# Kernel tuning notes

Hardware: AMD Instinct MI355X
Metric: run time of the kernel (lower is better)

## Reference

```python
import jax, jax.numpy as jnp
import numpy as np

B, L, D = 2048, 200, 256
N_USERS, N_ATTRS, N_RATINGS = 100000, 50000, 5


def setup_inputs() -> dict:
    key = jax.random.key(0)
    ks = jax.random.split(key, 16)
    s = 0.02
    return {
        "nodes": jax.random.randint(ks[0], (B,), 0, N_USERS),
        "history_ua": jax.random.randint(ks[1], (B, L), 0, N_ATTRS),
        "history_r": jax.random.randint(ks[2], (B, L), 0, N_RATINGS),
        "history_uat": jax.random.randint(ks[3], (B, L), 0, 512),
        "u2e_w": jax.random.normal(ks[4], (N_USERS, D), jnp.float32) * s,
        "attr_w": jax.random.normal(ks[5], (N_ATTRS, D), jnp.float32) * s,
        "r2e_w": jax.random.normal(ks[6], (N_RATINGS, D), jnp.float32) * s,
        "w_r1_w": jax.random.normal(ks[7], (D, 2 * D), jnp.float32) * s,
        "w_r1_b": jnp.zeros((D,), jnp.float32),
        "w_r2_w": jax.random.normal(ks[8], (D, D), jnp.float32) * s,
        "w_r2_b": jnp.zeros((D,), jnp.float32),
        "att1_w": jax.random.normal(ks[9], (D, 2 * D), jnp.float32) * s,
        "att1_b": jnp.zeros((D,), jnp.float32),
        "att2_w": jax.random.normal(ks[10], (D, D), jnp.float32) * s,
        "att2_b": jnp.zeros((D,), jnp.float32),
        "att3_w": jax.random.normal(ks[11], (1, D), jnp.float32) * s,
        "att3_b": jnp.zeros((1,), jnp.float32),
    }


def reference(nodes, history_ua, history_r, history_uat,
              u2e_w, attr_w, r2e_w,
              w_r1_w, w_r1_b, w_r2_w, w_r2_b,
              att1_w, att1_b, att2_w, att2_b, att3_w, att3_b):
    # gathers: e_ua [B,L,D], e_r [B,L,D], ua_rep [B,D]
    e_ua = attr_w[history_ua]
    e_r = r2e_w[history_r]
    ua_rep = u2e_w[nodes]
    # o_history = relu(w_r2(relu(w_r1(cat(e_ua, e_r)))))  [B,L,D]
    x = jnp.concatenate([e_ua, e_r], axis=-1)            # [B,L,2D]
    x = jax.nn.relu(jnp.einsum('bld,kd->blk', x, w_r1_w) + w_r1_b)
    o = jax.nn.relu(jnp.einsum('bld,kd->blk', x, w_r2_w) + w_r2_b)
    # attention: MLP on cat(o_history, ua_rep) -> softmax over history dim
    a = jnp.concatenate([o, jnp.broadcast_to(ua_rep[:, None, :], o.shape)], axis=-1)  # [B,L,2D]
    h = jax.nn.relu(jnp.einsum('bld,kd->blk', a, att1_w) + att1_b)
    h = jax.nn.relu(jnp.einsum('bld,kd->blk', h, att2_w) + att2_b)
    score = jnp.einsum('bld,kd->blk', h, att3_w) + att3_b  # [B,L,1]
    att = jax.nn.softmax(score, axis=1)
    # weighted reduce: o^T @ att per node -> [B,D]
    return jnp.sum(o * att, axis=1)
```

## Files before the change

### kernel.cpp

```cpp
#include <hip/hip_runtime.h>
#include <hip/hip_bf16.h>

typedef __bf16 bf16;
typedef __bf16 bf16x8 __attribute__((ext_vector_type(8)));
typedef float f32x4 __attribute__((ext_vector_type(4)));

#define L_SZ 200
#define D_SZ 256
#define NROWS (2048 * 200)
#define MB 128
#define AST 264
#define N_ATTR 50000

#define WS_W2F 0u
#define WS_A1L 131072u
#define WS_A1H 262144u
#define WS_A2F 393216u
#define WS_W1A 524288u
#define WS_W1F 655360u
#define WS_R   917504u
#define WS_H1P 925696u
#define WS_SCR 3022848u
#define WS_O   4661248u
#define WS_P   214376448u
#define WS_NEED_OLD 214376448u
#define WS_NEED_NEW 239976448u

__global__ void swizzle_kernel(const float* __restrict__ W, bf16* __restrict__ dst,
                               int KT, int ldw, int koff, int total) {
    int g = blockIdx.x * blockDim.x + threadIdx.x;
    if (g >= total) return;
    int lane = g & 63;
    int kt = (g >> 6) % KT;
    int nt = g / (64 * KT);
    int n = nt * 16 + (lane & 15);
    int k = kt * 32 + (lane >> 4) * 8;
    const float* src = W + (long)n * ldw + koff + k;
    f32x4 a = *(const f32x4*)src;
    f32x4 b = *(const f32x4*)(src + 4);
    bf16x8 v;
    v[0] = (bf16)a[0]; v[1] = (bf16)a[1]; v[2] = (bf16)a[2]; v[3] = (bf16)a[3];
    v[4] = (bf16)b[0]; v[5] = (bf16)b[1]; v[6] = (bf16)b[2]; v[7] = (bf16)b[3];
    *(bf16x8*)(dst + (long)g * 8) = v;
}

__device__ __forceinline__ void stage_rows(const int* __restrict__ idxl,
                                           const float* __restrict__ table,
                                           bf16* __restrict__ buf, int t) {
#pragma unroll
    for (int it = 0; it < 16; ++it) {
        int g = it * 256 + t;
        int r = g >> 5;
        int c = g & 31;
        long row = idxl[r];
        const float* f = table + row * D_SZ + c * 8;
        f32x4 a = *(const f32x4*)f;
        f32x4 b = *(const f32x4*)(f + 4);
        bf16x8 v;
        v[0] = (bf16)a[0]; v[1] = (bf16)a[1]; v[2] = (bf16)a[2]; v[3] = (bf16)a[3];
        v[4] = (bf16)b[0]; v[5] = (bf16)b[1]; v[6] = (bf16)b[2]; v[7] = (bf16)b[3];
        *(bf16x8*)(buf + r * AST + c * 8) = v;
    }
}

template <int KTOT>
__device__ __forceinline__ void gemm8(const bf16* __restrict__ abase,
                                      const bf16* __restrict__ wfrag, int koff_t,
                                      int wave, int lane, int l16, int quad,
                                      f32x4 acc[8][4]) {
    const bf16* wbase = wfrag + ((long)(wave * 4) * KTOT + koff_t) * 512 + lane * 8;
    bf16x8 bc[4], bn[4];
#pragma unroll
    for (int nt = 0; nt < 4; ++nt)
        bc[nt] = *(const bf16x8*)(wbase + (long)nt * KTOT * 512);
#pragma unroll
    for (int kt = 0; kt < 8; ++kt) {
        if (kt < 7) {
#pragma unroll
            for (int nt = 0; nt < 4; ++nt)
                bn[nt] = *(const bf16x8*)(wbase + ((long)nt * KTOT + kt + 1) * 512);
        }
        bf16x8 a[8];
#pragma unroll
        for (int mt = 0; mt < 8; ++mt)
            a[mt] = *(const bf16x8*)(abase + (mt * 16 + l16) * AST + kt * 32 + quad * 8);
#pragma unroll
        for (int nt = 0; nt < 4; ++nt)
#pragma unroll
            for (int mt = 0; mt < 8; ++mt)
                acc[mt][nt] = __builtin_amdgcn_mfma_f32_16x16x32_bf16(a[mt], bc[nt], acc[mt][nt], 0, 0, 0);
#pragma unroll
        for (int nt = 0; nt < 4; ++nt) bc[nt] = bn[nt];
    }
}

__device__ __forceinline__ void zero8(f32x4 acc[8][4]) {
    f32x4 z = {0.f, 0.f, 0.f, 0.f};
#pragma unroll
    for (int mt = 0; mt < 8; ++mt)
#pragma unroll
        for (int nt = 0; nt < 4; ++nt) acc[mt][nt] = z;
}

__device__ __forceinline__ void store_act8(bf16* __restrict__ buf, f32x4 acc[8][4],
                                           const float* bias, int wave, int l16, int quad) {
#pragma unroll
    for (int mt = 0; mt < 8; ++mt)
#pragma unroll
        for (int nt = 0; nt < 4; ++nt) {
            int col = (wave * 4 + nt) * 16 + l16;
#pragma unroll
            for (int r = 0; r < 4; ++r) {
                int row = mt * 16 + quad * 4 + r;
                float v = acc[mt][nt][r] + bias[nt];
                v = v > 0.f ? v : 0.f;
                buf[row * AST + col] = (bf16)v;
            }
        }
}

__device__ __forceinline__ void store_lin8(bf16* __restrict__ buf, f32x4 acc[8][4],
                                           int wave, int l16, int quad) {
#pragma unroll
    for (int mt = 0; mt < 8; ++mt)
#pragma unroll
        for (int nt = 0; nt < 4; ++nt) {
            int col = (wave * 4 + nt) * 16 + l16;
#pragma unroll
            for (int r = 0; r < 4; ++r) {
                int row = mt * 16 + quad * 4 + r;
                buf[row * AST + col] = (bf16)acc[mt][nt][r];
            }
        }
}

__global__ void kR_bias(const float* __restrict__ w1, const float* __restrict__ r2e,
                        const float* __restrict__ b1w, float* __restrict__ Rg) {
    __shared__ float e[5 * D_SZ];
    const int t = threadIdx.x;
    for (int i = t; i < 5 * D_SZ; i += 256) e[i] = r2e[i];
    __syncthreads();
    const float* wr = w1 + (long)t * 512 + 256;
    float bb = b1w[t];
    for (int r = 0; r < 5; ++r) {
        float a = bb;
        const float* er = e + r * D_SZ;
#pragma unroll
        for (int k = 0; k < D_SZ; k += 4) {
            f32x4 wv = *(const f32x4*)(wr + k);
            a += er[k] * wv[0] + er[k + 1] * wv[1] + er[k + 2] * wv[2] + er[k + 3] * wv[3];
        }
        Rg[r * D_SZ + t] = a;
    }
}

__launch_bounds__(256, 2)
__global__ void kpre_P(const float* __restrict__ attr, const bf16* __restrict__ wf_w1a,
                       bf16* __restrict__ Pt) {
    __shared__ __align__(16) bf16 abuf[MB * AST];
    __shared__ int idxl[MB];
    const int blk = blockIdx.x, t = threadIdx.x;
    const int wave = t >> 6, lane = t & 63, l16 = t & 15, quad = (t & 63) >> 4;
    if (t < MB) { int r = blk * MB + t; idxl[t] = r < N_ATTR ? r : (N_ATTR - 1); }
    __syncthreads();
    stage_rows(idxl, attr, abuf, t);
    __syncthreads();
    f32x4 acc[8][4];
    zero8(acc);
    gemm8<8>(abuf, wf_w1a, 0, wave, lane, l16, quad, acc);
    __syncthreads();
    store_lin8(abuf, acc, wave, l16, quad);
    __syncthreads();
#pragma unroll
    for (int it = 0; it < 16; ++it) {
        int g = it * 256 + t;
        int r = g >> 5, c = g & 31;
        long row = (long)blk * MB + r;
        if (row < N_ATTR)
            *(bf16x8*)(Pt + row * D_SZ + c * 8) = *(const bf16x8*)(abuf + r * AST + c * 8);
    }
}

__launch_bounds__(256, 2)
__global__ void k0_h1pre(const int* __restrict__ nodes, const float* __restrict__ u2e,
                         const bf16* __restrict__ wf_a1h, const float* __restrict__ a1b,
                         float* __restrict__ h1p) {
    __shared__ __align__(16) bf16 abuf[MB * AST];
    __shared__ int idxl[MB];
    const int blk = blockIdx.x, t = threadIdx.x;
    const int wave = t >> 6, lane = t & 63, l16 = t & 15, quad = (t & 63) >> 4;
    if (t < MB) idxl[t] = nodes[blk * MB + t];
    __syncthreads();
    stage_rows(idxl, u2e, abuf, t);
    __syncthreads();
    f32x4 acc[8][4];
    zero8(acc);
    gemm8<8>(abuf, wf_a1h, 0, wave, lane, l16, quad, acc);
#pragma unroll
    for (int nt = 0; nt < 4; ++nt) {
        int col = (wave * 4 + nt) * 16 + l16;
        float ab = a1b[col];
#pragma unroll
        for (int mt = 0; mt < 8; ++mt)
#pragma unroll
            for (int r = 0; r < 4; ++r) {
                int row = mt * 16 + quad * 4 + r;
                h1p[(long)(blk * MB + row) * D_SZ + col] = acc[mt][nt][r] + ab;
            }
    }
}

__launch_bounds__(256, 2)
__global__ void k1f_fused(const int* __restrict__ hua, const int* __restrict__ hr,
                          const bf16* __restrict__ Pt, const float* __restrict__ Rg,
                          const bf16* __restrict__ wf_w2, const bf16* __restrict__ wf_a1l,
                          const bf16* __restrict__ wf_a2f, const float* __restrict__ h1p,
                          const float* __restrict__ b2w, const float* __restrict__ a2b,
                          const float* __restrict__ a3w,
                          bf16* __restrict__ o_out, float* __restrict__ scores) {
    __shared__ __align__(16) bf16 abuf[MB * AST];
    __shared__ int idx_ua[MB], idx_r[MB];
    __shared__ float Rl[5 * D_SZ];
    __shared__ float hp[2][D_SZ];
    __shared__ float spart[4][MB];
    const int blk = blockIdx.x, t = threadIdx.x;
    const int wave = t >> 6, lane = t & 63, l16 = t & 15, quad = (t & 63) >> 4;
    const long r0 = (long)blk * MB;
    const int b0 = (int)(r0 / L_SZ);
    const int b1i = min(b0 + 1, 2047);
    const long bsplit = (long)(b0 + 1) * L_SZ;
    if (t < MB) { idx_ua[t] = hua[r0 + t]; idx_r[t] = hr[r0 + t]; }
    for (int i = t; i < 5 * D_SZ; i += 256) Rl[i] = Rg[i];
    hp[0][t] = h1p[(long)b0 * D_SZ + t];
    hp[1][t] = h1p[(long)b1i * D_SZ + t];
    __syncthreads();
#pragma unroll
    for (int it = 0; it < 8; ++it) {
        int g = it * 256 + t;
        int r = g >> 4, c = g & 15;
        long row = idx_ua[r];
        const bf16* pp = Pt + row * D_SZ + c * 16;
        bf16x8 v0 = *(const bf16x8*)pp;
        bf16x8 v1 = *(const bf16x8*)(pp + 8);
        const float* Rr = Rl + idx_r[r] * D_SZ + c * 16;
        f32x4 ra = *(const f32x4*)(Rr);
        f32x4 rb = *(const f32x4*)(Rr + 4);
        f32x4 rc = *(const f32x4*)(Rr + 8);
        f32x4 rd = *(const f32x4*)(Rr + 12);
        bf16x8 o0, o1;
#pragma unroll
        for (int j = 0; j < 4; ++j) {
            float a = (float)v0[j] + ra[j];
            float b = (float)v0[j + 4] + rb[j];
            float cc = (float)v1[j] + rc[j];
            float d = (float)v1[j + 4] + rd[j];
            o0[j]     = (bf16)(a > 0.f ? a : 0.f);
            o0[j + 4] = (bf16)(b > 0.f ? b : 0.f);
            o1[j]     = (bf16)(cc > 0.f ? cc : 0.f);
            o1[j + 4] = (bf16)(d > 0.f ? d : 0.f);
        }
        *(bf16x8*)(abuf + r * AST + c * 16) = o0;
        *(bf16x8*)(abuf + r * AST + c * 16 + 8) = o1;
    }
    __syncthreads();

    float bias2[4], bias4[4], a3[4];
#pragma unroll
    for (int nt = 0; nt < 4; ++nt) {
        int col = (wave * 4 + nt) * 16 + l16;
        bias2[nt] = b2w[col];
        bias4[nt] = a2b[col];
        a3[nt] = a3w[col];
    }

    f32x4 acc[8][4];
    zero8(acc);
    gemm8<8>(abuf, wf_w2, 0, wave, lane, l16, quad, acc);
    __syncthreads();
    store_act8(abuf, acc, bias2, wave, l16, quad);
    __syncthreads();
#pragma unroll
    for (int it = 0; it < 16; ++it) {
        int g = it * 256 + t;
        int r = g >> 5, c = g & 31;
        *(bf16x8*)(o_out + (r0 + r) * D_SZ + c * 8) = *(const bf16x8*)(abuf + r * AST + c * 8);
    }
    zero8(acc);
    gemm8<8>(abuf, wf_a1l, 0, wave, lane, l16, quad, acc);
    __syncthreads();
#pragma unroll
    for (int nt = 0; nt < 4; ++nt) {
        int col = (wave * 4 + nt) * 16 + l16;
#pragma unroll
        for (int mt = 0; mt < 8; ++mt)
#pragma unroll
            for (int r = 0; r < 4; ++r) {
                int row = mt * 16 + quad * 4 + r;
                float bias = ((r0 + row) >= bsplit) ? hp[1][col] : hp[0][col];
                float v = acc[mt][nt][r] + bias;
                v = v > 0.f ? v : 0.f;
                abuf[row * AST + col] = (bf16)v;
            }
    }
    __syncthreads();
    zero8(acc);
    gemm8<8>(abuf, wf_a2f, 0, wave, lane, l16, quad, acc);

    float p[8][4];
#pragma unroll
    for (int mt = 0; mt < 8; ++mt)
#pragma unroll
        for (int r = 0; r < 4; ++r) {
            float s = 0.f;
#pragma unroll
            for (int nt = 0; nt < 4; ++nt) {
                float h = acc[mt][nt][r] + bias4[nt];
                h = h > 0.f ? h : 0.f;
                s += h * a3[nt];
            }
            p[mt][r] = s;
        }
#pragma unroll
    for (int off = 1; off < 16; off <<= 1)
#pragma unroll
        for (int mt = 0; mt < 8; ++mt)
#pragma unroll
            for (int r = 0; r < 4; ++r) p[mt][r] += __shfl_xor(p[mt][r], off, 16);
    if (l16 == 0) {
#pragma unroll
        for (int mt = 0; mt < 8; ++mt)
#pragma unroll
            for (int r = 0; r < 4; ++r)
                spart[wave][mt * 16 + quad * 4 + r] = p[mt][r];
    }
    __syncthreads();
    if (t < MB)
        scores[r0 + t] = spart[0][t] + spart[1][t] + spart[2][t] + spart[3][t];
}

__launch_bounds__(256, 2)
__global__ void k1_gemm12(const int* __restrict__ hua, const int* __restrict__ hr,
                          const float* __restrict__ attr, const float* __restrict__ r2e,
                          const bf16* __restrict__ wf_w1, const bf16* __restrict__ wf_w2,
                          const float* __restrict__ b1w, const float* __restrict__ b2w,
                          bf16* __restrict__ o_out) {
    __shared__ __align__(16) bf16 abuf[MB * AST];
    __shared__ int idx_ua[MB], idx_r[MB];
    const int blk = blockIdx.x, t = threadIdx.x;
    const int wave = t >> 6, lane = t & 63, l16 = t & 15, quad = (t & 63) >> 4;
    const long r0 = (long)blk * MB;
    if (t < MB) { idx_ua[t] = hua[r0 + t]; idx_r[t] = hr[r0 + t]; }
    __syncthreads();

    float bias1[4], bias2[4];
#pragma unroll
    for (int nt = 0; nt < 4; ++nt) {
        int col = (wave * 4 + nt) * 16 + l16;
        bias1[nt] = b1w[col];
        bias2[nt] = b2w[col];
    }

    f32x4 acc[8][4];
    zero8(acc);
    stage_rows(idx_ua, attr, abuf, t);
    __syncthreads();
    gemm8<16>(abuf, wf_w1, 0, wave, lane, l16, quad, acc);
    __syncthreads();
    stage_rows(idx_r, r2e, abuf, t);
    __syncthreads();
    gemm8<16>(abuf, wf_w1, 8, wave, lane, l16, quad, acc);
    __syncthreads();
    store_act8(abuf, acc, bias1, wave, l16, quad);
    __syncthreads();
    zero8(acc);
    gemm8<8>(abuf, wf_w2, 0, wave, lane, l16, quad, acc);
    __syncthreads();
    store_act8(abuf, acc, bias2, wave, l16, quad);
    __syncthreads();
#pragma unroll
    for (int it = 0; it < 16; ++it) {
        int g = it * 256 + t;
        int r = g >> 5, c = g & 31;
        *(bf16x8*)(o_out + (r0 + r) * D_SZ + c * 8) = *(const bf16x8*)(abuf + r * AST + c * 8);
    }
}

__launch_bounds__(256, 2)
__global__ void k2_gemm34(const bf16* __restrict__ o_in,
                          const bf16* __restrict__ wf_a1l, const bf16* __restrict__ wf_a2f,
                          const float* __restrict__ h1p, const float* __restrict__ a2b,
                          const float* __restrict__ a3w, float* __restrict__ scores) {
    __shared__ __align__(16) bf16 abuf[MB * AST];
    __shared__ float hp[2][D_SZ];
    __shared__ float spart[4][MB];
    const int blk = blockIdx.x, t = threadIdx.x;
    const int wave = t >> 6, lane = t & 63, l16 = t & 15, quad = (t & 63) >> 4;
    const long r0 = (long)blk * MB;
    const int b0 = (int)(r0 / L_SZ);
    const int b1 = min(b0 + 1, 2047);
    const long bsplit = (long)(b0 + 1) * L_SZ;
    hp[0][t] = h1p[(long)b0 * D_SZ + t];
    hp[1][t] = h1p[(long)b1 * D_SZ + t];
#pragma unroll
    for (int it = 0; it < 16; ++it) {
        int g = it * 256 + t;
        int r = g >> 5, c = g & 31;
        *(bf16x8*)(abuf + r * AST + c * 8) = *(const bf16x8*)(o_in + (r0 + r) * D_SZ + c * 8);
    }
    __syncthreads();

    f32x4 acc[8][4];
    zero8(acc);
    gemm8<8>(abuf, wf_a1l, 0, wave, lane, l16, quad, acc);
    __syncthreads();
#pragma unroll
    for (int nt = 0; nt < 4; ++nt) {
        int col = (wave * 4 + nt) * 16 + l16;
#pragma unroll
        for (int mt = 0; mt < 8; ++mt)
#pragma unroll
            for (int r = 0; r < 4; ++r) {
                int row = mt * 16 + quad * 4 + r;
                float bias = ((r0 + row) >= bsplit) ? hp[1][col] : hp[0][col];
                float v = acc[mt][nt][r] + bias;
                v = v > 0.f ? v : 0.f;
                abuf[row * AST + col] = (bf16)v;
            }
    }
    __syncthreads();
    zero8(acc);
    gemm8<8>(abuf, wf_a2f, 0, wave, lane, l16, quad, acc);

    float bias4[4], a3[4];
#pragma unroll
    for (int nt = 0; nt < 4; ++nt) {
        int col = (wave * 4 + nt) * 16 + l16;
        bias4[nt] = a2b[col];
        a3[nt] = a3w[col];
    }
    float p[8][4];
#pragma unroll
    for (int mt = 0; mt < 8; ++mt)
#pragma unroll
        for (int r = 0; r < 4; ++r) {
            float s = 0.f;
#pragma unroll
            for (int nt = 0; nt < 4; ++nt) {
                float h = acc[mt][nt][r] + bias4[nt];
                h = h > 0.f ? h : 0.f;
                s += h * a3[nt];
            }
            p[mt][r] = s;
        }
#pragma unroll
    for (int off = 1; off < 16; off <<= 1)
#pragma unroll
        for (int mt = 0; mt < 8; ++mt)
#pragma unroll
            for (int r = 0; r < 4; ++r) p[mt][r] += __shfl_xor(p[mt][r], off, 16);
    if (l16 == 0) {
#pragma unroll
        for (int mt = 0; mt < 8; ++mt)
#pragma unroll
            for (int r = 0; r < 4; ++r)
                spart[wave][mt * 16 + quad * 4 + r] = p[mt][r];
    }
    __syncthreads();
    if (t < MB)
        scores[r0 + t] = spart[0][t] + spart[1][t] + spart[2][t] + spart[3][t];
}

__global__ void k5_reduce(const float* __restrict__ scores, const bf16* __restrict__ o_in,
                          float* __restrict__ out) {
    __shared__ float red[256];
    __shared__ float watt[256];
    const int b = blockIdx.x, t = threadIdx.x;
    float s = (t < L_SZ) ? scores[(long)b * L_SZ + t] : -INFINITY;
    red[t] = s;
    __syncthreads();
    for (int off = 128; off > 0; off >>= 1) {
        if (t < off) red[t] = fmaxf(red[t], red[t + off]);
        __syncthreads();
    }
    float mx = red[0];
    __syncthreads();
    float w = (t < L_SZ) ? __expf(s - mx) : 0.f;
    watt[t] = w;
    red[t] = w;
    __syncthreads();
    for (int off = 128; off > 0; off >>= 1) {
        if (t < off) red[t] += red[t + off];
        __syncthreads();
    }
    float inv = 1.f / red[0];
    float accv = 0.f;
    const bf16* ob = o_in + (long)b * L_SZ * D_SZ + t;
#pragma unroll 4
    for (int l = 0; l < L_SZ; ++l) accv += watt[l] * (float)ob[(long)l * D_SZ];
    out[(long)b * D_SZ + t] = accv * inv;
}

__device__ __forceinline__ void gather_half_f(const int* __restrict__ idxp,
                                              const float* __restrict__ table,
                                              bf16* __restrict__ buf, int l0, int t) {
#pragma unroll
    for (int it = 0; it < 6; ++it) {
        int g = it * 256 + t;
        int r = g >> 5, c = g & 31;
        int l = l0 + r;
        int li = l < L_SZ ? l : (L_SZ - 1);
        long row = idxp[li];
        const float* f = table + row * D_SZ + c * 8;
        f32x4 a = *(const f32x4*)f;
        f32x4 b2 = *(const f32x4*)(f + 4);
        bf16x8 v;
        v[0] = (bf16)a[0]; v[1] = (bf16)a[1]; v[2] = (bf16)a[2]; v[3] = (bf16)a[3];
        v[4] = (bf16)b2[0]; v[5] = (bf16)b2[1]; v[6] = (bf16)b2[2]; v[7] = (bf16)b2[3];
        *(bf16x8*)(buf + r * AST + c * 8) = v;
    }
}

template <int KTOT>
__device__ __forceinline__ void run_gemm3(const bf16* __restrict__ abase,
                                          const bf16* __restrict__ wfrag, int koff_t,
                                          int wave, int lane, int l16, int quad,
                                          f32x4 acc[3][4]) {
    const bf16* wbase = wfrag + ((long)(wave * 4) * KTOT + koff_t) * 512 + lane * 8;
    bf16x8 bc[4], bn[4];
#pragma unroll
    for (int nt = 0; nt < 4; ++nt)
        bc[nt] = *(const bf16x8*)(wbase + (long)nt * KTOT * 512);
#pragma unroll
    for (int kt = 0; kt < 8; ++kt) {
        if (kt < 7) {
#pragma unroll
            for (int nt = 0; nt < 4; ++nt)
                bn[nt] = *(const bf16x8*)(wbase + ((long)nt * KTOT + kt + 1) * 512);
        }
        bf16x8 a[3];
#pragma unroll
        for (int mt = 0; mt < 3; ++mt)
            a[mt] = *(const bf16x8*)(abase + (mt * 16 + l16) * AST + kt * 32 + quad * 8);
#pragma unroll
        for (int nt = 0; nt < 4; ++nt)
#pragma unroll
            for (int mt = 0; mt < 3; ++mt)
                acc[mt][nt] = __builtin_amdgcn_mfma_f32_16x16x32_bf16(a[mt], bc[nt], acc[mt][nt], 0, 0, 0);
#pragma unroll
        for (int nt = 0; nt < 4; ++nt) bc[nt] = bn[nt];
    }
}

__launch_bounds__(256, 3)
__global__ void ua_fused(const int* __restrict__ nodes, const int* __restrict__ hua,
                         const int* __restrict__ hr, const float* __restrict__ u2e,
                         const float* __restrict__ attr, const float* __restrict__ r2e,
                         const bf16* __restrict__ wf1, const bf16* __restrict__ wf2,
                         const bf16* __restrict__ wfa1, const bf16* __restrict__ wfa2,
                         const float* __restrict__ b1w, const float* __restrict__ b2w,
                         const float* __restrict__ att1w, const float* __restrict__ a1b,
                         const float* __restrict__ a2b, const float* __restrict__ att3w,
                         const float* __restrict__ a3bp, float* __restrict__ out) {
    __shared__ __align__(16) bf16 abuf[48 * AST];
    __shared__ __align__(16) bf16 obuf[48 * AST];
    __shared__ float h1pre[D_SZ];
    __shared__ float scratch[288];
    const int b = blockIdx.x, t = threadIdx.x;
    const int wave = t >> 6, lane = t & 63, l16 = t & 15, quad = (t & 63) >> 4;
    {
        int node = nodes[b];
        scratch[t] = u2e[(long)node * D_SZ + t];
        __syncthreads();
        float a = a1b[t];
        const float* wr = att1w + (long)t * 512 + 256;
#pragma unroll
        for (int k = 0; k < 256; k += 4) {
            f32x4 wv = *(const f32x4*)(wr + k);
            a += scratch[k] * wv[0] + scratch[k + 1] * wv[1] +
                 scratch[k + 2] * wv[2] + scratch[k + 3] * wv[3];
        }
        h1pre[t] = a;
        __syncthreads();
    }
    float bias1[4], bias2[4], bias3[4], bias4[4], a3[4];
#pragma unroll
    for (int nt = 0; nt < 4; ++nt) {
        int col = (wave * 4 + nt) * 16 + l16;
        bias1[nt] = b1w[col]; bias2[nt] = b2w[col]; bias3[nt] = h1pre[col];
        bias4[nt] = a2b[col]; a3[nt] = att3w[col];
    }
    const float a3bias = a3bp[0];
    const int* huab = hua + (long)b * L_SZ;
    const int* hrb = hr + (long)b * L_SZ;
    float accv = 0.f, srun = 0.f, mrun = -INFINITY;
    float* score_part = scratch;
    float* score_row = scratch + 192;
    float* wrow = scratch + 240;
    auto st3 = [&](bf16* buf, f32x4 acc[3][4], const float* bias) {
#pragma unroll
        for (int mt = 0; mt < 3; ++mt)
#pragma unroll
            for (int nt = 0; nt < 4; ++nt) {
                int col = (wave * 4 + nt) * 16 + l16;
#pragma unroll
                for (int r = 0; r < 4; ++r) {
                    float v = acc[mt][nt][r] + bias[nt];
                    v = v > 0.f ? v : 0.f;
                    buf[(mt * 16 + quad * 4 + r) * AST + col] = (bf16)v;
                }
            }
    };
    for (int tile = 0; tile < 5; ++tile) {
        const int l0 = tile * 48;
        f32x4 acc[3][4];
        f32x4 z = {0.f, 0.f, 0.f, 0.f};
#pragma unroll
        for (int mt = 0; mt < 3; ++mt)
#pragma unroll
            for (int nt = 0; nt < 4; ++nt) acc[mt][nt] = z;
        gather_half_f(huab, attr, abuf, l0, t);
        __syncthreads();
        run_gemm3<16>(abuf, wf1, 0, wave, lane, l16, quad, acc);
        __syncthreads();
        gather_half_f(hrb, r2e, abuf, l0, t);
        __syncthreads();
        run_gemm3<16>(abuf, wf1, 8, wave, lane, l16, quad, acc);
        __syncthreads();
        st3(abuf, acc, bias1);
        __syncthreads();
#pragma unroll
        for (int mt = 0; mt < 3; ++mt)
#pragma unroll
            for (int nt = 0; nt < 4; ++nt) acc[mt][nt] = z;
        run_gemm3<8>(abuf, wf2, 0, wave, lane, l16, quad, acc);
        st3(obuf, acc, bias2);
        __syncthreads();
#pragma unroll
        for (int mt = 0; mt < 3; ++mt)
#pragma unroll
            for (int nt = 0; nt < 4; ++nt) acc[mt][nt] = z;
        run_gemm3<8>(obuf, wfa1, 0, wave, lane, l16, quad, acc);
        st3(abuf, acc, bias3);
        __syncthreads();
#pragma unroll
        for (int mt = 0; mt < 3; ++mt)
#pragma unroll
            for (int nt = 0; nt < 4; ++nt) acc[mt][nt] = z;
        run_gemm3<8>(abuf, wfa2, 0, wave, lane, l16, quad, acc);
        float p[3][4];
#pragma unroll
        for (int mt = 0; mt < 3; ++mt)
#pragma unroll
            for (int r = 0; r < 4; ++r) {
                float s = 0.f;
#pragma unroll
                for (int nt = 0; nt < 4; ++nt) {
                    float h = acc[mt][nt][r] + bias4[nt];
                    h = h > 0.f ? h : 0.f;
                    s += h * a3[nt];
                }
                p[mt][r] = s;
            }
#pragma unroll
        for (int off = 1; off < 16; off <<= 1)
#pragma unroll
            for (int mt = 0; mt < 3; ++mt)
#pragma unroll
                for (int r = 0; r < 4; ++r) p[mt][r] += __shfl_xor(p[mt][r], off, 16);
        if (l16 == 0) {
#pragma unroll
            for (int mt = 0; mt < 3; ++mt)
#pragma unroll
                for (int r = 0; r < 4; ++r)
                    score_part[wave * 48 + mt * 16 + quad * 4 + r] = p[mt][r];
        }
        __syncthreads();
        if (t < 48) {
            float s = score_part[t] + score_part[48 + t] + score_part[96 + t] +
                      score_part[144 + t] + a3bias;
            score_row[t] = (l0 + t < L_SZ) ? s : -INFINITY;
        }
        __syncthreads();
        float tm = -INFINITY;
        for (int r = 0; r < 48; ++r) tm = fmaxf(tm, score_row[r]);
        float nm = fmaxf(mrun, tm);
        float factor = __expf(mrun - nm);
        if (t < 48) wrow[t] = __expf(score_row[t] - nm);
        __syncthreads();
        float wsum = 0.f, av = 0.f;
#pragma unroll 8
        for (int r = 0; r < 48; ++r) {
            float w = wrow[r];
            wsum += w;
            av += w * (float)obuf[r * AST + t];
        }
        accv = accv * factor + av;
        srun = srun * factor + wsum;
        mrun = nm;
        __syncthreads();
    }
    out[(long)b * D_SZ + t] = accv / srun;
}

extern "C" void kernel_launch(void* const* d_in, const int* in_sizes, int n_in,
                              void* d_out, int out_size, void* d_ws, size_t ws_size,
                              hipStream_t stream) {
    const int* nodes = (const int*)d_in[0];
    const int* hua = (const int*)d_in[1];
    const int* hr = (const int*)d_in[2];
    const float* u2e = (const float*)d_in[4];
    const float* attr = (const float*)d_in[5];
    const float* r2e = (const float*)d_in[6];
    const float* w1 = (const float*)d_in[7];
    const float* b1 = (const float*)d_in[8];
    const float* w2 = (const float*)d_in[9];
    const float* b2 = (const float*)d_in[10];
    const float* a1w = (const float*)d_in[11];
    const float* a1b = (const float*)d_in[12];
    const float* a2w = (const float*)d_in[13];
    const float* a2b = (const float*)d_in[14];
    const float* a3w = (const float*)d_in[15];
    const float* a3b = (const float*)d_in[16];
    char* ws = (char*)d_ws;
    bf16* wf_w2 = (bf16*)(ws + WS_W2F);
    bf16* wf_a1l = (bf16*)(ws + WS_A1L);
    bf16* wf_a1h = (bf16*)(ws + WS_A1H);
    bf16* wf_a2f = (bf16*)(ws + WS_A2F);
    bf16* wf_w1a = (bf16*)(ws + WS_W1A);
    bf16* wf_w1 = (bf16*)(ws + WS_W1F);

    swizzle_kernel<<<32, 256, 0, stream>>>(w2, wf_w2, 8, 256, 0, 8192);
    swizzle_kernel<<<32, 256, 0, stream>>>(a1w, wf_a1l, 8, 512, 0, 8192);
    swizzle_kernel<<<32, 256, 0, stream>>>(a2w, wf_a2f, 8, 256, 0, 8192);

    if (ws_size >= (size_t)WS_NEED_NEW) {
        float* Rg = (float*)(ws + WS_R);
        float* h1p = (float*)(ws + WS_H1P);
        float* scores = (float*)(ws + WS_SCR);
        bf16* obuf = (bf16*)(ws + WS_O);
        bf16* Pt = (bf16*)(ws + WS_P);
        swizzle_kernel<<<32, 256, 0, stream>>>(a1w, wf_a1h, 8, 512, 256, 8192);
        swizzle_kernel<<<32, 256, 0, stream>>>(w1, wf_w1a, 8, 512, 0, 8192);
        kR_bias<<<1, 256, 0, stream>>>(w1, r2e, b1, Rg);
        kpre_P<<<(N_ATTR + MB - 1) / MB, 256, 0, stream>>>(attr, wf_w1a, Pt);
        k0_h1pre<<<2048 / MB, 256, 0, stream>>>(nodes, u2e, wf_a1h, a1b, h1p);
        k1f_fused<<<NROWS / MB, 256, 0, stream>>>(hua, hr, Pt, Rg, wf_w2, wf_a1l,
                                                  wf_a2f, h1p, b2, a2b, a3w,
                                                  obuf, scores);
        k5_reduce<<<2048, 256, 0, stream>>>(scores, obuf, (float*)d_out);
    } else if (ws_size >= (size_t)WS_NEED_OLD) {
        float* h1p = (float*)(ws + WS_H1P);
        float* scores = (float*)(ws + WS_SCR);
        bf16* obuf = (bf16*)(ws + WS_O);
        swizzle_kernel<<<64, 256, 0, stream>>>(w1, wf_w1, 16, 512, 0, 16384);
        swizzle_kernel<<<32, 256, 0, stream>>>(a1w, wf_a1h, 8, 512, 256, 8192);
        k0_h1pre<<<2048 / MB, 256, 0, stream>>>(nodes, u2e, wf_a1h, a1b, h1p);
        k1_gemm12<<<NROWS / MB, 256, 0, stream>>>(hua, hr, attr, r2e, wf_w1, wf_w2,
                                                  b1, b2, obuf);
        k2_gemm34<<<NROWS / MB, 256, 0, stream>>>(obuf, wf_a1l, wf_a2f, h1p, a2b,
                                                  a3w, scores);
        k5_reduce<<<2048, 256, 0, stream>>>(scores, obuf, (float*)d_out);
    } else {
        swizzle_kernel<<<64, 256, 0, stream>>>(w1, wf_w1, 16, 512, 0, 16384);
        ua_fused<<<2048, 256, 0, stream>>>(nodes, hua, hr, u2e, attr, r2e,
                                           wf_w1, wf_w2, wf_a1l, wf_a2f,
                                           b1, b2, a1w, a1b, a2b, a3w, a3b,
                                           (float*)d_out);
    }
}
```

Baseline: 614.6 us.

## Halve fused tile rows, merge prep kernels, and vectorize the weighted reduce

The main fused kernel now processes 64 rows per block instead of 128, with launch bounds raised to 4 blocks per CU. This shrinks LDS and accumulator registers so more blocks can be resident. The five swizzle launches and the R-bias kernel are merged into one launch, and the P-precompute and user-projection kernels are merged into another, cutting launch overhead. The final reduce reads bf16x8 vectors across 8 row groups and combines them through shared memory, replacing the strided scalar loads. Smaller tiles mean each weight fragment is reused over fewer rows, so weight traffic per output row doubles.

```diff
diff --git a/kernel.cpp b/kernel.cpp
--- a/kernel.cpp
+++ b/kernel.cpp
@@ -9,8 +9,10 @@
 #define D_SZ 256
 #define NROWS (2048 * 200)
 #define MB 128
+#define MB2 64
 #define AST 264
 #define N_ATTR 50000
+#define NPB ((N_ATTR + MB - 1) / MB)
 
 #define WS_W2F 0u
 #define WS_A1L 131072u
@@ -26,10 +28,8 @@
 #define WS_NEED_OLD 214376448u
 #define WS_NEED_NEW 239976448u
 
-__global__ void swizzle_kernel(const float* __restrict__ W, bf16* __restrict__ dst,
-                               int KT, int ldw, int koff, int total) {
-    int g = blockIdx.x * blockDim.x + threadIdx.x;
-    if (g >= total) return;
+__device__ __forceinline__ void swz_one(const float* __restrict__ W, bf16* __restrict__ dst,
+                                        int KT, int ldw, int koff, int g) {
     int lane = g & 63;
     int kt = (g >> 6) % KT;
     int nt = g / (64 * KT);
@@ -44,6 +44,52 @@
     *(bf16x8*)(dst + (long)g * 8) = v;
 }
 
+__global__ void swizzle_kernel(const float* __restrict__ W, bf16* __restrict__ dst,
+                               int KT, int ldw, int koff, int total) {
+    int g = blockIdx.x * blockDim.x + threadIdx.x;
+    if (g >= total) return;
+    swz_one(W, dst, KT, ldw, koff, g);
+}
+
+__global__ void swizzle_all(const float* __restrict__ w2, const float* __restrict__ a1w,
+                            const float* __restrict__ a2w, const float* __restrict__ w1,
+                            bf16* __restrict__ wf_w2, bf16* __restrict__ wf_a1l,
+                            bf16* __restrict__ wf_a2f, bf16* __restrict__ wf_a1h,
+                            bf16* __restrict__ wf_w1a,
+                            const float* __restrict__ r2e, const float* __restrict__ b1w,
+                            float* __restrict__ Rg) {
+    __shared__ float e[5 * D_SZ];
+    const int blk = blockIdx.x, t = threadIdx.x;
+    if (blk == 160) {
+        for (int i = t; i < 5 * D_SZ; i += 256) e[i] = r2e[i];
+        __syncthreads();
+        const float* wr = w1 + (long)t * 512 + 256;
+        float bb = b1w[t];
+        for (int r = 0; r < 5; ++r) {
+            float a = bb;
+            const float* er = e + r * D_SZ;
+#pragma unroll
+            for (int k = 0; k < D_SZ; k += 4) {
+                f32x4 wv = *(const f32x4*)(wr + k);
+                a += er[k] * wv[0] + er[k + 1] * wv[1] + er[k + 2] * wv[2] + er[k + 3] * wv[3];
+            }
+            Rg[r * D_SZ + t] = a;
+        }
+        return;
+    }
+    int job = blk >> 5, lb = blk & 31;
+    int g = lb * 256 + t;
+    const float* W; bf16* dst; int ldw, koff;
+    switch (job) {
+        case 0:  W = w2;  dst = wf_w2;  ldw = 256; koff = 0;   break;
+        case 1:  W = a1w; dst = wf_a1l; ldw = 512; koff = 0;   break;
+        case 2:  W = a2w; dst = wf_a2f; ldw = 256; koff = 0;   break;
+        case 3:  W = a1w; dst = wf_a1h; ldw = 512; koff = 256; break;
+        default: W = w1;  dst = wf_w1a; ldw = 512; koff = 0;   break;
+    }
+    swz_one(W, dst, 8, ldw, koff, g);
+}
+
 __device__ __forceinline__ void stage_rows(const int* __restrict__ idxl,
                                            const float* __restrict__ table,
                                            bf16* __restrict__ buf, int t) {
@@ -63,11 +109,11 @@
     }
 }
 
-template <int KTOT>
-__device__ __forceinline__ void gemm8(const bf16* __restrict__ abase,
-                                      const bf16* __restrict__ wfrag, int koff_t,
-                                      int wave, int lane, int l16, int quad,
-                                      f32x4 acc[8][4]) {
+template <int MT, int KTOT>
+__device__ __forceinline__ void gemm_t(const bf16* __restrict__ abase,
+                                       const bf16* __restrict__ wfrag, int koff_t,
+                                       int wave, int lane, int l16, int quad,
+                                       f32x4 (&acc)[MT][4]) {
     const bf16* wbase = wfrag + ((long)(wave * 4) * KTOT + koff_t) * 512 + lane * 8;
     bf16x8 bc[4], bn[4];
 #pragma unroll
@@ -80,32 +126,34 @@
             for (int nt = 0; nt < 4; ++nt)
                 bn[nt] = *(const bf16x8*)(wbase + ((long)nt * KTOT + kt + 1) * 512);
         }
-        bf16x8 a[8];
-#pragma unroll
-        for (int mt = 0; mt < 8; ++mt)
+        bf16x8 a[MT];
+#pragma unroll
+        for (int mt = 0; mt < MT; ++mt)
             a[mt] = *(const bf16x8*)(abase + (mt * 16 + l16) * AST + kt * 32 + quad * 8);
 #pragma unroll
         for (int nt = 0; nt < 4; ++nt)
 #pragma unroll
-            for (int mt = 0; mt < 8; ++mt)
+            for (int mt = 0; mt < MT; ++mt)
                 acc[mt][nt] = __builtin_amdgcn_mfma_f32_16x16x32_bf16(a[mt], bc[nt], acc[mt][nt], 0, 0, 0);
 #pragma unroll
         for (int nt = 0; nt < 4; ++nt) bc[nt] = bn[nt];
     }
 }
 
-__device__ __forceinline__ void zero8(f32x4 acc[8][4]) {
+template <int MT>
+__device__ __forceinline__ void zero_t(f32x4 (&acc)[MT][4]) {
     f32x4 z = {0.f, 0.f, 0.f, 0.f};
 #pragma unroll
-    for (int mt = 0; mt < 8; ++mt)
+    for (int mt = 0; mt < MT; ++mt)
 #pragma unroll
         for (int nt = 0; nt < 4; ++nt) acc[mt][nt] = z;
 }
 
-__device__ __forceinline__ void store_act8(bf16* __restrict__ buf, f32x4 acc[8][4],
-                                           const float* bias, int wave, int l16, int quad) {
-#pragma unroll
-    for (int mt = 0; mt < 8; ++mt)
+template <int MT>
+__device__ __forceinline__ void store_act_t(bf16* __restrict__ buf, f32x4 (&acc)[MT][4],
+                                            const float* bias, int wave, int l16, int quad) {
+#pragma unroll
+    for (int mt = 0; mt < MT; ++mt)
 #pragma unroll
         for (int nt = 0; nt < 4; ++nt) {
             int col = (wave * 4 + nt) * 16 + l16;
@@ -119,7 +167,7 @@
         }
 }
 
-__device__ __forceinline__ void store_lin8(bf16* __restrict__ buf, f32x4 acc[8][4],
+__device__ __forceinline__ void store_lin8(bf16* __restrict__ buf, f32x4 (&acc)[8][4],
                                            int wave, int l16, int quad) {
 #pragma unroll
     for (int mt = 0; mt < 8; ++mt)
@@ -134,50 +182,53 @@
         }
 }
 
-__global__ void kR_bias(const float* __restrict__ w1, const float* __restrict__ r2e,
-                        const float* __restrict__ b1w, float* __restrict__ Rg) {
-    __shared__ float e[5 * D_SZ];
-    const int t = threadIdx.x;
-    for (int i = t; i < 5 * D_SZ; i += 256) e[i] = r2e[i];
-    __syncthreads();
-    const float* wr = w1 + (long)t * 512 + 256;
-    float bb = b1w[t];
-    for (int r = 0; r < 5; ++r) {
-        float a = bb;
-        const float* er = e + r * D_SZ;
-#pragma unroll
-        for (int k = 0; k < D_SZ; k += 4) {
-            f32x4 wv = *(const f32x4*)(wr + k);
-            a += er[k] * wv[0] + er[k + 1] * wv[1] + er[k + 2] * wv[2] + er[k + 3] * wv[3];
-        }
-        Rg[r * D_SZ + t] = a;
-    }
-}
-
 __launch_bounds__(256, 2)
-__global__ void kpre_P(const float* __restrict__ attr, const bf16* __restrict__ wf_w1a,
-                       bf16* __restrict__ Pt) {
+__global__ void kpre_k0(const float* __restrict__ attr, const bf16* __restrict__ wf_w1a,
+                        bf16* __restrict__ Pt,
+                        const int* __restrict__ nodes, const float* __restrict__ u2e,
+                        const bf16* __restrict__ wf_a1h, const float* __restrict__ a1b,
+                        float* __restrict__ h1p) {
     __shared__ __align__(16) bf16 abuf[MB * AST];
     __shared__ int idxl[MB];
     const int blk = blockIdx.x, t = threadIdx.x;
     const int wave = t >> 6, lane = t & 63, l16 = t & 15, quad = (t & 63) >> 4;
-    if (t < MB) { int r = blk * MB + t; idxl[t] = r < N_ATTR ? r : (N_ATTR - 1); }
-    __syncthreads();
-    stage_rows(idxl, attr, abuf, t);
+    const bool isP = blk < NPB;
+    if (t < MB) {
+        if (isP) { int r = blk * MB + t; idxl[t] = r < N_ATTR ? r : (N_ATTR - 1); }
+        else idxl[t] = nodes[(blk - NPB) * MB + t];
+    }
+    __syncthreads();
+    stage_rows(idxl, isP ? attr : u2e, abuf, t);
     __syncthreads();
     f32x4 acc[8][4];
-    zero8(acc);
-    gemm8<8>(abuf, wf_w1a, 0, wave, lane, l16, quad, acc);
-    __syncthreads();
-    store_lin8(abuf, acc, wave, l16, quad);
-    __syncthreads();
-#pragma unroll
-    for (int it = 0; it < 16; ++it) {
-        int g = it * 256 + t;
-        int r = g >> 5, c = g & 31;
-        long row = (long)blk * MB + r;
-        if (row < N_ATTR)
-            *(bf16x8*)(Pt + row * D_SZ + c * 8) = *(const bf16x8*)(abuf + r * AST + c * 8);
+    zero_t<8>(acc);
+    gemm_t<8, 8>(abuf, isP ? wf_w1a : wf_a1h, 0, wave, lane, l16, quad, acc);
+    if (isP) {
+        __syncthreads();
+        store_lin8(abuf, acc, wave, l16, quad);
+        __syncthreads();
+#pragma unroll
+        for (int it = 0; it < 16; ++it) {
+            int g = it * 256 + t;
+            int r = g >> 5, c = g & 31;
+            long row = (long)blk * MB + r;
+            if (row < N_ATTR)
+                *(bf16x8*)(Pt + row * D_SZ + c * 8) = *(const bf16x8*)(abuf + r * AST + c * 8);
+        }
+    } else {
+        const int blk0 = blk - NPB;
+#pragma unroll
+        for (int nt = 0; nt < 4; ++nt) {
+            int col = (wave * 4 + nt) * 16 + l16;
+            float ab = a1b[col];
+#pragma unroll
+            for (int mt = 0; mt < 8; ++mt)
+#pragma unroll
+                for (int r = 0; r < 4; ++r) {
+                    int row = mt * 16 + quad * 4 + r;
+                    h1p[(long)(blk0 * MB + row) * D_SZ + col] = acc[mt][nt][r] + ab;
+                }
+        }
     }
 }
 
@@ -194,8 +245,8 @@
     stage_rows(idxl, u2e, abuf, t);
     __syncthreads();
     f32x4 acc[8][4];
-    zero8(acc);
-    gemm8<8>(abuf, wf_a1h, 0, wave, lane, l16, quad, acc);
+    zero_t<8>(acc);
+    gemm_t<8, 8>(abuf, wf_a1h, 0, wave, lane, l16, quad, acc);
 #pragma unroll
     for (int nt = 0; nt < 4; ++nt) {
         int col = (wave * 4 + nt) * 16 + l16;
@@ -210,7 +261,7 @@
     }
 }
 
-__launch_bounds__(256, 2)
+__launch_bounds__(256, 4)
 __global__ void k1f_fused(const int* __restrict__ hua, const int* __restrict__ hr,
                           const bf16* __restrict__ Pt, const float* __restrict__ Rg,
                           const bf16* __restrict__ wf_w2, const bf16* __restrict__ wf_a1l,
@@ -218,24 +269,21 @@
                           const float* __restrict__ b2w, const float* __restrict__ a2b,
                           const float* __restrict__ a3w,
                           bf16* __restrict__ o_out, float* __restrict__ scores) {
-    __shared__ __align__(16) bf16 abuf[MB * AST];
-    __shared__ int idx_ua[MB], idx_r[MB];
+    __shared__ __align__(16) bf16 abuf[MB2 * AST];
+    __shared__ int idx_ua[MB2], idx_r[MB2];
     __shared__ float Rl[5 * D_SZ];
-    __shared__ float hp[2][D_SZ];
-    __shared__ float spart[4][MB];
+    __shared__ float spart[4][MB2];
     const int blk = blockIdx.x, t = threadIdx.x;
     const int wave = t >> 6, lane = t & 63, l16 = t & 15, quad = (t & 63) >> 4;
-    const long r0 = (long)blk * MB;
+    const long r0 = (long)blk * MB2;
     const int b0 = (int)(r0 / L_SZ);
     const int b1i = min(b0 + 1, 2047);
     const long bsplit = (long)(b0 + 1) * L_SZ;
-    if (t < MB) { idx_ua[t] = hua[r0 + t]; idx_r[t] = hr[r0 + t]; }
+    if (t < MB2) { idx_ua[t] = hua[r0 + t]; idx_r[t] = hr[r0 + t]; }
     for (int i = t; i < 5 * D_SZ; i += 256) Rl[i] = Rg[i];
-    hp[0][t] = h1p[(long)b0 * D_SZ + t];
-    hp[1][t] = h1p[(long)b1i * D_SZ + t];
-    __syncthreads();
-#pragma unroll
-    for (int it = 0; it < 8; ++it) {
+    __syncthreads();
+#pragma unroll
+    for (int it = 0; it < 4; ++it) {
         int g = it * 256 + t;
         int r = g >> 4, c = g & 15;
         long row = idx_ua[r];
@@ -264,51 +312,59 @@
     }
     __syncthreads();
 
-    float bias2[4], bias4[4], a3[4];
-#pragma unroll
-    for (int nt = 0; nt < 4; ++nt) {
-        int col = (wave * 4 + nt) * 16 + l16;
-        bias2[nt] = b2w[col];
-        bias4[nt] = a2b[col];
-        a3[nt] = a3w[col];
-    }
-
-    f32x4 acc[8][4];
-    zero8(acc);
-    gemm8<8>(abuf, wf_w2, 0, wave, lane, l16, quad, acc);
-    __syncthreads();
-    store_act8(abuf, acc, bias2, wave, l16, quad);
-    __syncthreads();
-#pragma unroll
-    for (int it = 0; it < 16; ++it) {
+    f32x4 acc[4][4];
+    zero_t<4>(acc);
+    gemm_t<4, 8>(abuf, wf_w2, 0, wave, lane, l16, quad, acc);
+    __syncthreads();
+    float bias2[4];
+#pragma unroll
+    for (int nt = 0; nt < 4; ++nt) bias2[nt] = b2w[(wave * 4 + nt) * 16 + l16];
+    store_act_t<4>(abuf, acc, bias2, wave, l16, quad);
+    __syncthreads();
+#pragma unroll
+    for (int it = 0; it < 8; ++it) {
         int g = it * 256 + t;
         int r = g >> 5, c = g & 31;
         *(bf16x8*)(o_out + (r0 + r) * D_SZ + c * 8) = *(const bf16x8*)(abuf + r * AST + c * 8);
     }
-    zero8(acc);
-    gemm8<8>(abuf, wf_a1l, 0, wave, lane, l16, quad, acc);
-    __syncthreads();
+    zero_t<4>(acc);
+    gemm_t<4, 8>(abuf, wf_a1l, 0, wave, lane, l16, quad, acc);
+    __syncthreads();
+    float h0v[4], h1v[4];
 #pragma unroll
     for (int nt = 0; nt < 4; ++nt) {
         int col = (wave * 4 + nt) * 16 + l16;
-#pragma unroll
-        for (int mt = 0; mt < 8; ++mt)
+        h0v[nt] = h1p[(long)b0 * D_SZ + col];
+        h1v[nt] = h1p[(long)b1i * D_SZ + col];
+    }
+#pragma unroll
+    for (int nt = 0; nt < 4; ++nt) {
+        int col = (wave * 4 + nt) * 16 + l16;
+#pragma unroll
+        for (int mt = 0; mt < 4; ++mt)
 #pragma unroll
             for (int r = 0; r < 4; ++r) {
                 int row = mt * 16 + quad * 4 + r;
-                float bias = ((r0 + row) >= bsplit) ? hp[1][col] : hp[0][col];
+                float bias = ((r0 + row) >= bsplit) ? h1v[nt] : h0v[nt];
                 float v = acc[mt][nt][r] + bias;
                 v = v > 0.f ? v : 0.f;
                 abuf[row * AST + col] = (bf16)v;
             }
     }
     __syncthreads();
-    zero8(acc);
-    gemm8<8>(abuf, wf_a2f, 0, wave, lane, l16, quad, acc);
-
-    float p[8][4];
-#pragma unroll
-    for (int mt = 0; mt < 8; ++mt)
+    zero_t<4>(acc);
+    gemm_t<4, 8>(abuf, wf_a2f, 0, wave, lane, l16, quad, acc);
+
+    float bias4[4], a3[4];
+#pragma unroll
+    for (int nt = 0; nt < 4; ++nt) {
+        int col = (wave * 4 + nt) * 16 + l16;
+        bias4[nt] = a2b[col];
+        a3[nt] = a3w[col];
+    }
+    float p[4][4];
+#pragma unroll
+    for (int mt = 0; mt < 4; ++mt)
 #pragma unroll
         for (int r = 0; r < 4; ++r) {
             float s = 0.f;
@@ -323,18 +379,18 @@
 #pragma unroll
     for (int off = 1; off < 16; off <<= 1)
 #pragma unroll
-        for (int mt = 0; mt < 8; ++mt)
+        for (int mt = 0; mt < 4; ++mt)
 #pragma unroll
             for (int r = 0; r < 4; ++r) p[mt][r] += __shfl_xor(p[mt][r], off, 16);
     if (l16 == 0) {
 #pragma unroll
-        for (int mt = 0; mt < 8; ++mt)
+        for (int mt = 0; mt < 4; ++mt)
 #pragma unroll
             for (int r = 0; r < 4; ++r)
                 spart[wave][mt * 16 + quad * 4 + r] = p[mt][r];
     }
     __syncthreads();
-    if (t < MB)
+    if (t < MB2)
         scores[r0 + t] = spart[0][t] + spart[1][t] + spart[2][t] + spart[3][t];
 }
 
@@ -361,21 +417,21 @@
     }
 
     f32x4 acc[8][4];
-    zero8(acc);
+    zero_t<8>(acc);
     stage_rows(idx_ua, attr, abuf, t);
     __syncthreads();
-    gemm8<16>(abuf, wf_w1, 0, wave, lane, l16, quad, acc);
+    gemm_t<8, 16>(abuf, wf_w1, 0, wave, lane, l16, quad, acc);
     __syncthreads();
     stage_rows(idx_r, r2e, abuf, t);
     __syncthreads();
-    gemm8<16>(abuf, wf_w1, 8, wave, lane, l16, quad, acc);
-    __syncthreads();
-    store_act8(abuf, acc, bias1, wave, l16, quad);
-    __syncthreads();
-    zero8(acc);
-    gemm8<8>(abuf, wf_w2, 0, wave, lane, l16, quad, acc);
-    __syncthreads();
-    store_act8(abuf, acc, bias2, wave, l16, quad);
+    gemm_t<8, 16>(abuf, wf_w1, 8, wave, lane, l16, quad, acc);
+    __syncthreads();
+    store_act_t<8>(abuf, acc, bias1, wave, l16, quad);
+    __syncthreads();
+    zero_t<8>(acc);
+    gemm_t<8, 8>(abuf, wf_w2, 0, wave, lane, l16, quad, acc);
+    __syncthreads();
+    store_act_t<8>(abuf, acc, bias2, wave, l16, quad);
     __syncthreads();
 #pragma unroll
     for (int it = 0; it < 16; ++it) {
@@ -410,8 +466,8 @@
     __syncthreads();
 
     f32x4 acc[8][4];
-    zero8(acc);
-    gemm8<8>(abuf, wf_a1l, 0, wave, lane, l16, quad, acc);
+    zero_t<8>(acc);
+    gemm_t<8, 8>(abuf, wf_a1l, 0, wave, lane, l16, quad, acc);
     __syncthreads();
 #pragma unroll
     for (int nt = 0; nt < 4; ++nt) {
@@ -428,8 +484,8 @@
             }
     }
     __syncthreads();
-    zero8(acc);
-    gemm8<8>(abuf, wf_a2f, 0, wave, lane, l16, quad, acc);
+    zero_t<8>(acc);
+    gemm_t<8, 8>(abuf, wf_a2f, 0, wave, lane, l16, quad, acc);
 
     float bias4[4], a3[4];
 #pragma unroll
@@ -474,6 +530,7 @@
                           float* __restrict__ out) {
     __shared__ float red[256];
     __shared__ float watt[256];
+    __shared__ float racc[8][264];
     const int b = blockIdx.x, t = threadIdx.x;
     float s = (t < L_SZ) ? scores[(long)b * L_SZ + t] : -INFINITY;
     red[t] = s;
@@ -493,11 +550,25 @@
         __syncthreads();
     }
     float inv = 1.f / red[0];
-    float accv = 0.f;
-    const bf16* ob = o_in + (long)b * L_SZ * D_SZ + t;
-#pragma unroll 4
-    for (int l = 0; l < L_SZ; ++l) accv += watt[l] * (float)ob[(long)l * D_SZ];
-    out[(long)b * D_SZ + t] = accv * inv;
+    const int c8 = t & 31, rg = t >> 5;
+    f32x4 a0 = {0.f, 0.f, 0.f, 0.f}, a1 = {0.f, 0.f, 0.f, 0.f};
+    const bf16* ob = o_in + (long)b * L_SZ * D_SZ + c8 * 8;
+#pragma unroll 5
+    for (int l = rg; l < L_SZ; l += 8) {
+        float wv = watt[l];
+        bf16x8 v = *(const bf16x8*)(ob + (long)l * D_SZ);
+        a0[0] += wv * (float)v[0]; a0[1] += wv * (float)v[1];
+        a0[2] += wv * (float)v[2]; a0[3] += wv * (float)v[3];
+        a1[0] += wv * (float)v[4]; a1[1] += wv * (float)v[5];
+        a1[2] += wv * (float)v[6]; a1[3] += wv * (float)v[7];
+    }
+    *(f32x4*)(&racc[rg][c8 * 8]) = a0;
+    *(f32x4*)(&racc[rg][c8 * 8 + 4]) = a1;
+    __syncthreads();
+    float r2 = 0.f;
+#pragma unroll
+    for (int g = 0; g < 8; ++g) r2 += racc[g][t];
+    out[(long)b * D_SZ + t] = r2 * inv;
 }
 
 __device__ __forceinline__ void gather_half_f(const int* __restrict__ idxp,
@@ -517,37 +588,6 @@
         v[0] = (bf16)a[0]; v[1] = (bf16)a[1]; v[2] = (bf16)a[2]; v[3] = (bf16)a[3];
         v[4] = (bf16)b2[0]; v[5] = (bf16)b2[1]; v[6] = (bf16)b2[2]; v[7] = (bf16)b2[3];
         *(bf16x8*)(buf + r * AST + c * 8) = v;
-    }
-}
-
-template <int KTOT>
-__device__ __forceinline__ void run_gemm3(const bf16* __restrict__ abase,
-                                          const bf16* __restrict__ wfrag, int koff_t,
-                                          int wave, int lane, int l16, int quad,
-                                          f32x4 acc[3][4]) {
-    const bf16* wbase = wfrag + ((long)(wave * 4) * KTOT + koff_t) * 512 + lane * 8;
-    bf16x8 bc[4], bn[4];
-#pragma unroll
-    for (int nt = 0; nt < 4; ++nt)
-        bc[nt] = *(const bf16x8*)(wbase + (long)nt * KTOT * 512);
-#pragma unroll
-    for (int kt = 0; kt < 8; ++kt) {
-        if (kt < 7) {
-#pragma unroll
-            for (int nt = 0; nt < 4; ++nt)
-                bn[nt] = *(const bf16x8*)(wbase + ((long)nt * KTOT + kt + 1) * 512);
-        }
-        bf16x8 a[3];
-#pragma unroll
-        for (int mt = 0; mt < 3; ++mt)
-            a[mt] = *(const bf16x8*)(abase + (mt * 16 + l16) * AST + kt * 32 + quad * 8);
-#pragma unroll
-        for (int nt = 0; nt < 4; ++nt)
-#pragma unroll
-            for (int mt = 0; mt < 3; ++mt)
-                acc[mt][nt] = __builtin_amdgcn_mfma_f32_16x16x32_bf16(a[mt], bc[nt], acc[mt][nt], 0, 0, 0);
-#pragma unroll
-        for (int nt = 0; nt < 4; ++nt) bc[nt] = bn[nt];
     }
 }
 
@@ -596,7 +636,7 @@
     float* score_part = scratch;
     float* score_row = scratch + 192;
     float* wrow = scratch + 240;
-    auto st3 = [&](bf16* buf, f32x4 acc[3][4], const float* bias) {
+    auto st3 = [&](bf16* buf, f32x4 (&acc)[3][4], const float* bias) {
 #pragma unroll
         for (int mt = 0; mt < 3; ++mt)
 #pragma unroll
@@ -613,40 +653,27 @@
     for (int tile = 0; tile < 5; ++tile) {
         const int l0 = tile * 48;
         f32x4 acc[3][4];
-        f32x4 z = {0.f, 0.f, 0.f, 0.f};
-#pragma unroll
-        for (int mt = 0; mt < 3; ++mt)
-#pragma unroll
-            for (int nt = 0; nt < 4; ++nt) acc[mt][nt] = z;
+        zero_t<3>(acc);
         gather_half_f(huab, attr, abuf, l0, t);
         __syncthreads();
-        run_gemm3<16>(abuf, wf1, 0, wave, lane, l16, quad, acc);
+        gemm_t<3, 16>(abuf, wf1, 0, wave, lane, l16, quad, acc);
         __syncthreads();
         gather_half_f(hrb, r2e, abuf, l0, t);
         __syncthreads();
-        run_gemm3<16>(abuf, wf1, 8, wave, lane, l16, quad, acc);
+        gemm_t<3, 16>(abuf, wf1, 8, wave, lane, l16, quad, acc);
         __syncthreads();
         st3(abuf, acc, bias1);
         __syncthreads();
-#pragma unroll
-        for (int mt = 0; mt < 3; ++mt)
-#pragma unroll
-            for (int nt = 0; nt < 4; ++nt) acc[mt][nt] = z;
-        run_gemm3<8>(abuf, wf2, 0, wave, lane, l16, quad, acc);
+        zero_t<3>(acc);
+        gemm_t<3, 8>(abuf, wf2, 0, wave, lane, l16, quad, acc);
         st3(obuf, acc, bias2);
         __syncthreads();
-#pragma unroll
-        for (int mt = 0; mt < 3; ++mt)
-#pragma unroll
-            for (int nt = 0; nt < 4; ++nt) acc[mt][nt] = z;
-        run_gemm3<8>(obuf, wfa1, 0, wave, lane, l16, quad, acc);
+        zero_t<3>(acc);
+        gemm_t<3, 8>(obuf, wfa1, 0, wave, lane, l16, quad, acc);
         st3(abuf, acc, bias3);
         __syncthreads();
-#pragma unroll
-        for (int mt = 0; mt < 3; ++mt)
-#pragma unroll
-            for (int nt = 0; nt < 4; ++nt) acc[mt][nt] = z;
-        run_gemm3<8>(abuf, wfa2, 0, wave, lane, l16, quad, acc);
+        zero_t<3>(acc);
+        gemm_t<3, 8>(abuf, wfa2, 0, wave, lane, l16, quad, acc);
         float p[3][4];
 #pragma unroll
         for (int mt = 0; mt < 3; ++mt)
@@ -729,29 +756,28 @@
     bf16* wf_w1a = (bf16*)(ws + WS_W1A);
     bf16* wf_w1 = (bf16*)(ws + WS_W1F);
 
-    swizzle_kernel<<<32, 256, 0, stream>>>(w2, wf_w2, 8, 256, 0, 8192);
-    swizzle_kernel<<<32, 256, 0, stream>>>(a1w, wf_a1l, 8, 512, 0, 8192);
-    swizzle_kernel<<<32, 256, 0, stream>>>(a2w, wf_a2f, 8, 256, 0, 8192);
-
     if (ws_size >= (size_t)WS_NEED_NEW) {
         float* Rg = (float*)(ws + WS_R);
         float* h1p = (float*)(ws + WS_H1P);
         float* scores = (float*)(ws + WS_SCR);
         bf16* obuf = (bf16*)(ws + WS_O);
         bf16* Pt = (bf16*)(ws + WS_P);
-        swizzle_kernel<<<32, 256, 0, stream>>>(a1w, wf_a1h, 8, 512, 256, 8192);
-        swizzle_kernel<<<32, 256, 0, stream>>>(w1, wf_w1a, 8, 512, 0, 8192);
-        kR_bias<<<1, 256, 0, stream>>>(w1, r2e, b1, Rg);
-        kpre_P<<<(N_ATTR + MB - 1) / MB, 256, 0, stream>>>(attr, wf_w1a, Pt);
-        k0_h1pre<<<2048 / MB, 256, 0, stream>>>(nodes, u2e, wf_a1h, a1b, h1p);
-        k1f_fused<<<NROWS / MB, 256, 0, stream>>>(hua, hr, Pt, Rg, wf_w2, wf_a1l,
-                                                  wf_a2f, h1p, b2, a2b, a3w,
-                                                  obuf, scores);
+        swizzle_all<<<161, 256, 0, stream>>>(w2, a1w, a2w, w1,
+                                             wf_w2, wf_a1l, wf_a2f, wf_a1h, wf_w1a,
+                                             r2e, b1, Rg);
+        kpre_k0<<<NPB + 2048 / MB, 256, 0, stream>>>(attr, wf_w1a, Pt,
+                                                     nodes, u2e, wf_a1h, a1b, h1p);
+        k1f_fused<<<NROWS / MB2, 256, 0, stream>>>(hua, hr, Pt, Rg, wf_w2, wf_a1l,
+                                                   wf_a2f, h1p, b2, a2b, a3w,
+                                                   obuf, scores);
         k5_reduce<<<2048, 256, 0, stream>>>(scores, obuf, (float*)d_out);
     } else if (ws_size >= (size_t)WS_NEED_OLD) {
         float* h1p = (float*)(ws + WS_H1P);
         float* scores = (float*)(ws + WS_SCR);
         bf16* obuf = (bf16*)(ws + WS_O);
+        swizzle_kernel<<<32, 256, 0, stream>>>(w2, wf_w2, 8, 256, 0, 8192);
+        swizzle_kernel<<<32, 256, 0, stream>>>(a1w, wf_a1l, 8, 512, 0, 8192);
+        swizzle_kernel<<<32, 256, 0, stream>>>(a2w, wf_a2f, 8, 256, 0, 8192);
         swizzle_kernel<<<64, 256, 0, stream>>>(w1, wf_w1, 16, 512, 0, 16384);
         swizzle_kernel<<<32, 256, 0, stream>>>(a1w, wf_a1h, 8, 512, 256, 8192);
         k0_h1pre<<<2048 / MB, 256, 0, stream>>>(nodes, u2e, wf_a1h, a1b, h1p);
@@ -761,6 +787,9 @@
                                                   a3w, scores);
         k5_reduce<<<2048, 256, 0, stream>>>(scores, obuf, (float*)d_out);
     } else {
+        swizzle_kernel<<<32, 256, 0, stream>>>(w2, wf_w2, 8, 256, 0, 8192);
+        swizzle_kernel<<<32, 256, 0, stream>>>(a1w, wf_a1l, 8, 512, 0, 8192);
+        swizzle_kernel<<<32, 256, 0, stream>>>(a2w, wf_a2f, 8, 256, 0, 8192);
         swizzle_kernel<<<64, 256, 0, stream>>>(w1, wf_w1, 16, 512, 0, 16384);
         ua_fused<<<2048, 256, 0, stream>>>(nodes, hua, hr, u2e, attr, r2e,
                                            wf_w1, wf_w2, wf_a1l, wf_a2f,
```

Result: faster. 526.5 us (-14.3%).
